# Performance work log

Hardware: AMD Instinct MI355X
Metric: run time of the kernel (lower is better)

## Reference

```python
import jax, jax.numpy as jnp
import numpy as np

E = 64          # num experts
CAP = 64        # tokens per expert (uniform routing)
H = 1024        # hidden_size
F = 2048        # ffn_hidden_size


def setup_inputs() -> dict:
    key = jax.random.key(0)
    k1, k2, k3 = jax.random.split(key, 3)
    x = jax.random.normal(k1, (E * CAP, H), dtype=jnp.float32)
    # dMoE stores expert weights flattened as [E*F, H]
    w1 = jax.random.normal(k2, (E * F, H), dtype=jnp.float32) * 0.02
    w2 = jax.random.normal(k3, (E * F, H), dtype=jnp.float32) * 0.02
    return {"x": x, "w1": w1, "w2": w2, "num_experts": E}


def reference(x, w1, w2, num_experts):
    # Block-sparse sdd/dsd over a block-diagonal expert topology is a grouped GEMM:
    # tokens are sorted by expert; each group of CAP tokens hits one expert's weights.
    T, Hd = x.shape
    Fd = w1.shape[0] // num_experts
    cap = T // num_experts
    xg = x.reshape(num_experts, cap, Hd)            # [E, cap, H]
    w1g = w1.reshape(num_experts, Fd, Hd)           # [E, F, H]
    w2g = w2.reshape(num_experts, Fd, Hd)           # [E, F, H]
    # sdd: x @ w1^T restricted to expert blocks
    h = jnp.einsum('ech,efh->ecf', xg, w1g)         # [E, cap, F]
    # megablocks' gelu kernel uses the tanh approximation
    h = jax.nn.gelu(h, approximate=True)
    # dsd: h @ w2 restricted to expert blocks
    out = jnp.einsum('ecf,efh->ech', h, w2g)        # [E, cap, H]
    return out.reshape(T, Hd)
```

## Files before the change

### kernel.cpp

```cpp
#include <hip/hip_runtime.h>


typedef __attribute__((ext_vector_type(8))) short short8;
typedef __attribute__((ext_vector_type(4))) float f32x4;
typedef __attribute__((ext_vector_type(8))) unsigned short ushort8;

#define NE   64
#define CAPT 64
#define HD   1024
#define FD   2048

__device__ __forceinline__ unsigned short f2bf(float f) {
  union { float f; unsigned u; } v; v.f = f;
  unsigned r = v.u + 0x7FFFu + ((v.u >> 16) & 1u);
  return (unsigned short)(r >> 16);
}

__device__ __forceinline__ float gelu_t(float v) {
  float u = 0.7978845608028654f * (v + 0.044715f * v * v * v);
  return 0.5f * v * (1.0f + tanhf(u));
}

__device__ __forceinline__ int swz(int row, int kbyte) {
  return row * 128 + (kbyte ^ ((row & 7) << 4));
}

__device__ __forceinline__ void cvt_wr4(unsigned char* dst, float4 v) {
  uint2 p;
  p.x = (unsigned)f2bf(v.x) | ((unsigned)f2bf(v.y) << 16);
  p.y = (unsigned)f2bf(v.z) | ((unsigned)f2bf(v.w) << 16);
  *(uint2*)dst = p;
}

__global__ __launch_bounds__(512, 4)
void moe_pass1(const float* __restrict__ x, const float* __restrict__ w1,
               unsigned short* __restrict__ hb) {
  __shared__ __align__(16) unsigned char sA[64 * 128];
  __shared__ __align__(16) unsigned char sB[128 * 128];
  const int e = blockIdx.x >> 4, nb = blockIdx.x & 15;
  const int t = threadIdx.x, lane = t & 63, wid = t >> 6;
  const int wm = wid >> 2, wn = wid & 3;
  const int lr = lane & 15, lkb = (lane >> 4) * 16;

  const float* xg  = x  + (size_t)e * CAPT * HD;
  const float* w1g = w1 + ((size_t)e * FD + (size_t)nb * 128) * HD;

  f32x4 acc[2][2] = {};

  float4 ra[2], rb[4];
  auto loadT = [&](int k0) {
    #pragma unroll
    for (int i = 0; i < 2; ++i) {
      int u = t + i * 512;
      ra[i] = *(const float4*)(xg + (u >> 4) * HD + k0 + (u & 15) * 4);
    }
    #pragma unroll
    for (int i = 0; i < 4; ++i) {
      int u = t + i * 512;
      rb[i] = *(const float4*)(w1g + (u >> 4) * HD + k0 + (u & 15) * 4);
    }
  };

  loadT(0);
  for (int ks = 0; ks < HD / 64; ++ks) {
    __syncthreads();
    #pragma unroll
    for (int i = 0; i < 2; ++i) {
      int u = t + i * 512;
      cvt_wr4(sA + swz(u >> 4, (u & 15) * 8), ra[i]);
    }
    #pragma unroll
    for (int i = 0; i < 4; ++i) {
      int u = t + i * 512;
      cvt_wr4(sB + swz(u >> 4, (u & 15) * 8), rb[i]);
    }
    __syncthreads();
    if (ks + 1 < HD / 64) loadT((ks + 1) * 64);

    short8 af[2][2], bf[2][2];
    #pragma unroll
    for (int fm = 0; fm < 2; ++fm)
      #pragma unroll
      for (int kk = 0; kk < 2; ++kk) {
        int row = wm * 32 + fm * 16 + lr;
        af[fm][kk] = *(const short8*)(sA + swz(row, kk * 64 + lkb));
      }
    #pragma unroll
    for (int fn = 0; fn < 2; ++fn)
      #pragma unroll
      for (int kk = 0; kk < 2; ++kk) {
        int row = wn * 32 + fn * 16 + lr;
        bf[fn][kk] = *(const short8*)(sB + swz(row, kk * 64 + lkb));
      }
    #pragma unroll
    for (int fm = 0; fm < 2; ++fm)
      #pragma unroll
      for (int fn = 0; fn < 2; ++fn) {
        acc[fm][fn] = __builtin_amdgcn_mfma_f32_16x16x32_bf16(af[fm][0], bf[fn][0], acc[fm][fn], 0, 0, 0);
        acc[fm][fn] = __builtin_amdgcn_mfma_f32_16x16x32_bf16(af[fm][1], bf[fn][1], acc[fm][fn], 0, 0, 0);
      }
  }

  unsigned short* hp = hb + (size_t)e * CAPT * FD + nb * 128;
  #pragma unroll
  for (int fm = 0; fm < 2; ++fm)
    #pragma unroll
    for (int fn = 0; fn < 2; ++fn)
      #pragma unroll
      for (int j = 0; j < 4; ++j) {
        int m = wm * 32 + fm * 16 + (lane >> 4) * 4 + j;
        int f = wn * 32 + fn * 16 + lr;
        hp[(size_t)m * FD + f] = f2bf(gelu_t(acc[fm][fn][j]));
      }
}

__global__ __launch_bounds__(512, 4)
void moe_pass2(const unsigned short* __restrict__ hb, const float* __restrict__ w2,
               float* __restrict__ out) {
  __shared__ __align__(16) unsigned char sA[64 * 128];
  __shared__ __align__(16) unsigned char sB[128 * 128];
  const int e = blockIdx.x >> 3, nb = blockIdx.x & 7;
  const int t = threadIdx.x, lane = t & 63, wid = t >> 6;
  const int wm = wid >> 2, wn = wid & 3;
  const int lr = lane & 15, lkb = (lane >> 4) * 16;

  const unsigned short* hg = hb + (size_t)e * CAPT * FD;
  const float* w2g = w2 + (size_t)e * FD * HD + nb * 128;

  f32x4 acc[2][2] = {};

  const int ar = t >> 3, ac = t & 7;
  const int bn = t & 127, bkg = t >> 7;

  ushort8 rav;
  float rbv[16];
  auto loadT = [&](int f0) {
    rav = *(const ushort8*)(hg + (size_t)ar * FD + f0 + ac * 8);
    #pragma unroll
    for (int i = 0; i < 4; ++i)
      #pragma unroll
      for (int j = 0; j < 4; ++j)
        rbv[i * 4 + j] = w2g[(size_t)(f0 + bkg * 16 + i * 4 + j) * HD + bn];
  };

  loadT(0);
  for (int ks = 0; ks < FD / 64; ++ks) {
    __syncthreads();
    *(ushort8*)(sA + swz(ar, ac * 16)) = rav;
    #pragma unroll
    for (int i = 0; i < 4; ++i) {
      uint2 p;
      p.x = (unsigned)f2bf(rbv[i * 4 + 0]) | ((unsigned)f2bf(rbv[i * 4 + 1]) << 16);
      p.y = (unsigned)f2bf(rbv[i * 4 + 2]) | ((unsigned)f2bf(rbv[i * 4 + 3]) << 16);
      *(uint2*)(sB + swz(bn, (bkg * 16 + i * 4) * 2)) = p;
    }
    __syncthreads();
    if (ks + 1 < FD / 64) loadT((ks + 1) * 64);

    short8 af[2][2], bf[2][2];
    #pragma unroll
    for (int fm = 0; fm < 2; ++fm)
      #pragma unroll
      for (int kk = 0; kk < 2; ++kk) {
        int row = wm * 32 + fm * 16 + lr;
        af[fm][kk] = *(const short8*)(sA + swz(row, kk * 64 + lkb));
      }
    #pragma unroll
    for (int fn = 0; fn < 2; ++fn)
      #pragma unroll
      for (int kk = 0; kk < 2; ++kk) {
        int row = wn * 32 + fn * 16 + lr;
        bf[fn][kk] = *(const short8*)(sB + swz(row, kk * 64 + lkb));
      }
    #pragma unroll
    for (int fm = 0; fm < 2; ++fm)
      #pragma unroll
      for (int fn = 0; fn < 2; ++fn) {
        acc[fm][fn] = __builtin_amdgcn_mfma_f32_16x16x32_bf16(af[fm][0], bf[fn][0], acc[fm][fn], 0, 0, 0);
        acc[fm][fn] = __builtin_amdgcn_mfma_f32_16x16x32_bf16(af[fm][1], bf[fn][1], acc[fm][fn], 0, 0, 0);
      }
  }

  float* op = out + (size_t)e * CAPT * HD + nb * 128;
  #pragma unroll
  for (int fm = 0; fm < 2; ++fm)
    #pragma unroll
    for (int fn = 0; fn < 2; ++fn)
      #pragma unroll
      for (int j = 0; j < 4; ++j) {
        int m = wm * 32 + fm * 16 + (lane >> 4) * 4 + j;
        int n = wn * 32 + fn * 16 + lr;
        op[(size_t)m * HD + n] = acc[fm][fn][j];
      }
}

extern "C" void kernel_launch(void* const* d_in, const int* in_sizes, int n_in,
                              void* d_out, int out_size, void* d_ws, size_t ws_size,
                              hipStream_t stream) {
  const float* x  = (const float*)d_in[0];
  const float* w1 = (const float*)d_in[1];
  const float* w2 = (const float*)d_in[2];
  float* out = (float*)d_out;
  unsigned short* hb = (unsigned short*)d_ws;
  (void)in_sizes; (void)n_in; (void)out_size; (void)ws_size;

  moe_pass1<<<dim3(NE * (FD / 128)), dim3(512), 0, stream>>>(x, w1, hb);
  moe_pass2<<<dim3(NE * (HD / 128)), dim3(512), 0, stream>>>(hb, w2, out);
}
```

Baseline: 234.3 us.

## Double-buffer LDS tiles in both GEMM passes and use an exp-based GELU

Both grouped-GEMM kernels now keep two LDS buffers. The next tile is converted and written to the idle buffer while MFMAs read the current one, so each k-step needs one barrier instead of two, and global loads are issued two steps ahead. The tanh GELU is rewritten algebraically as v*sigmoid(2u) using __expf, which is cheaper than tanhf. The cost is double the LDS per block (48KB), which may lower occupancy against the requested 4 blocks per CU, and more registers held live across iterations.

```diff
diff --git a/kernel.cpp b/kernel.cpp
--- a/kernel.cpp
+++ b/kernel.cpp
@@ -17,8 +17,8 @@
 }
 
 __device__ __forceinline__ float gelu_t(float v) {
-  float u = 0.7978845608028654f * (v + 0.044715f * v * v * v);
-  return 0.5f * v * (1.0f + tanhf(u));
+  float u = 1.5957691216057308f * (v + 0.044715f * v * v * v);
+  return v / (1.0f + __expf(-u));
 }
 
 __device__ __forceinline__ int swz(int row, int kbyte) {
@@ -32,11 +32,14 @@
   *(uint2*)dst = p;
 }
 
+#define A_SZ (64 * 128)
+#define B_SZ (128 * 128)
+
 __global__ __launch_bounds__(512, 4)
 void moe_pass1(const float* __restrict__ x, const float* __restrict__ w1,
                unsigned short* __restrict__ hb) {
-  __shared__ __align__(16) unsigned char sA[64 * 128];
-  __shared__ __align__(16) unsigned char sB[128 * 128];
+  __shared__ __align__(16) unsigned char sA[2 * A_SZ];
+  __shared__ __align__(16) unsigned char sB[2 * B_SZ];
   const int e = blockIdx.x >> 4, nb = blockIdx.x & 15;
   const int t = threadIdx.x, lane = t & 63, wid = t >> 6;
   const int wm = wid >> 2, wn = wid & 3;
@@ -60,38 +63,43 @@
       rb[i] = *(const float4*)(w1g + (u >> 4) * HD + k0 + (u & 15) * 4);
     }
   };
-
+  auto writeT = [&](unsigned char* a, unsigned char* b) {
+    #pragma unroll
+    for (int i = 0; i < 2; ++i) {
+      int u = t + i * 512;
+      cvt_wr4(a + swz(u >> 4, (u & 15) * 8), ra[i]);
+    }
+    #pragma unroll
+    for (int i = 0; i < 4; ++i) {
+      int u = t + i * 512;
+      cvt_wr4(b + swz(u >> 4, (u & 15) * 8), rb[i]);
+    }
+  };
+
+  const int NK = HD / 64;
   loadT(0);
-  for (int ks = 0; ks < HD / 64; ++ks) {
-    __syncthreads();
-    #pragma unroll
-    for (int i = 0; i < 2; ++i) {
-      int u = t + i * 512;
-      cvt_wr4(sA + swz(u >> 4, (u & 15) * 8), ra[i]);
-    }
-    #pragma unroll
-    for (int i = 0; i < 4; ++i) {
-      int u = t + i * 512;
-      cvt_wr4(sB + swz(u >> 4, (u & 15) * 8), rb[i]);
-    }
-    __syncthreads();
-    if (ks + 1 < HD / 64) loadT((ks + 1) * 64);
+  writeT(sA, sB);
+  loadT(64);
+  __syncthreads();
+
+  int cur = 0;
+  for (int ks = 0; ks < NK; ++ks) {
+    unsigned char* cA = sA + cur * A_SZ;
+    unsigned char* cB = sB + cur * B_SZ;
+    if (ks + 1 < NK) writeT(sA + (cur ^ 1) * A_SZ, sB + (cur ^ 1) * B_SZ);
+    if (ks + 2 < NK) loadT((ks + 2) * 64);
 
     short8 af[2][2], bf[2][2];
     #pragma unroll
     for (int fm = 0; fm < 2; ++fm)
       #pragma unroll
-      for (int kk = 0; kk < 2; ++kk) {
-        int row = wm * 32 + fm * 16 + lr;
-        af[fm][kk] = *(const short8*)(sA + swz(row, kk * 64 + lkb));
-      }
-    #pragma unroll
-    for (int fn = 0; fn < 2; ++fn)
-      #pragma unroll
-      for (int kk = 0; kk < 2; ++kk) {
-        int row = wn * 32 + fn * 16 + lr;
-        bf[fn][kk] = *(const short8*)(sB + swz(row, kk * 64 + lkb));
-      }
+      for (int kk = 0; kk < 2; ++kk)
+        af[fm][kk] = *(const short8*)(cA + swz(wm * 32 + fm * 16 + lr, kk * 64 + lkb));
+    #pragma unroll
+    for (int fn = 0; fn < 2; ++fn)
+      #pragma unroll
+      for (int kk = 0; kk < 2; ++kk)
+        bf[fn][kk] = *(const short8*)(cB + swz(wn * 32 + fn * 16 + lr, kk * 64 + lkb));
     #pragma unroll
     for (int fm = 0; fm < 2; ++fm)
       #pragma unroll
@@ -99,6 +107,8 @@
         acc[fm][fn] = __builtin_amdgcn_mfma_f32_16x16x32_bf16(af[fm][0], bf[fn][0], acc[fm][fn], 0, 0, 0);
         acc[fm][fn] = __builtin_amdgcn_mfma_f32_16x16x32_bf16(af[fm][1], bf[fn][1], acc[fm][fn], 0, 0, 0);
       }
+    __syncthreads();
+    cur ^= 1;
   }
 
   unsigned short* hp = hb + (size_t)e * CAPT * FD + nb * 128;
@@ -117,8 +127,8 @@
 __global__ __launch_bounds__(512, 4)
 void moe_pass2(const unsigned short* __restrict__ hb, const float* __restrict__ w2,
                float* __restrict__ out) {
-  __shared__ __align__(16) unsigned char sA[64 * 128];
-  __shared__ __align__(16) unsigned char sB[128 * 128];
+  __shared__ __align__(16) unsigned char sA[2 * A_SZ];
+  __shared__ __align__(16) unsigned char sB[2 * B_SZ];
   const int e = blockIdx.x >> 3, nb = blockIdx.x & 7;
   const int t = threadIdx.x, lane = t & 63, wid = t >> 6;
   const int wm = wid >> 2, wn = wid & 3;
@@ -142,36 +152,41 @@
       for (int j = 0; j < 4; ++j)
         rbv[i * 4 + j] = w2g[(size_t)(f0 + bkg * 16 + i * 4 + j) * HD + bn];
   };
-
-  loadT(0);
-  for (int ks = 0; ks < FD / 64; ++ks) {
-    __syncthreads();
-    *(ushort8*)(sA + swz(ar, ac * 16)) = rav;
+  auto writeT = [&](unsigned char* a, unsigned char* b) {
+    *(ushort8*)(a + swz(ar, ac * 16)) = rav;
     #pragma unroll
     for (int i = 0; i < 4; ++i) {
       uint2 p;
       p.x = (unsigned)f2bf(rbv[i * 4 + 0]) | ((unsigned)f2bf(rbv[i * 4 + 1]) << 16);
       p.y = (unsigned)f2bf(rbv[i * 4 + 2]) | ((unsigned)f2bf(rbv[i * 4 + 3]) << 16);
-      *(uint2*)(sB + swz(bn, (bkg * 16 + i * 4) * 2)) = p;
-    }
-    __syncthreads();
-    if (ks + 1 < FD / 64) loadT((ks + 1) * 64);
+      *(uint2*)(b + swz(bn, (bkg * 16 + i * 4) * 2)) = p;
+    }
+  };
+
+  const int NK = FD / 64;
+  loadT(0);
+  writeT(sA, sB);
+  loadT(64);
+  __syncthreads();
+
+  int cur = 0;
+  for (int ks = 0; ks < NK; ++ks) {
+    unsigned char* cA = sA + cur * A_SZ;
+    unsigned char* cB = sB + cur * B_SZ;
+    if (ks + 1 < NK) writeT(sA + (cur ^ 1) * A_SZ, sB + (cur ^ 1) * B_SZ);
+    if (ks + 2 < NK) loadT((ks + 2) * 64);
 
     short8 af[2][2], bf[2][2];
     #pragma unroll
     for (int fm = 0; fm < 2; ++fm)
       #pragma unroll
-      for (int kk = 0; kk < 2; ++kk) {
-        int row = wm * 32 + fm * 16 + lr;
-        af[fm][kk] = *(const short8*)(sA + swz(row, kk * 64 + lkb));
-      }
-    #pragma unroll
-    for (int fn = 0; fn < 2; ++fn)
-      #pragma unroll
-      for (int kk = 0; kk < 2; ++kk) {
-        int row = wn * 32 + fn * 16 + lr;
-        bf[fn][kk] = *(const short8*)(sB + swz(row, kk * 64 + lkb));
-      }
+      for (int kk = 0; kk < 2; ++kk)
+        af[fm][kk] = *(const short8*)(cA + swz(wm * 32 + fm * 16 + lr, kk * 64 + lkb));
+    #pragma unroll
+    for (int fn = 0; fn < 2; ++fn)
+      #pragma unroll
+      for (int kk = 0; kk < 2; ++kk)
+        bf[fn][kk] = *(const short8*)(cB + swz(wn * 32 + fn * 16 + lr, kk * 64 + lkb));
     #pragma unroll
     for (int fm = 0; fm < 2; ++fm)
       #pragma unroll
@@ -179,6 +194,8 @@
         acc[fm][fn] = __builtin_amdgcn_mfma_f32_16x16x32_bf16(af[fm][0], bf[fn][0], acc[fm][fn], 0, 0, 0);
         acc[fm][fn] = __builtin_amdgcn_mfma_f32_16x16x32_bf16(af[fm][1], bf[fn][1], acc[fm][fn], 0, 0, 0);
       }
+    __syncthreads();
+    cur ^= 1;
   }
 
   float* op = out + (size_t)e * CAPT * HD + nb * 128;
```

Result: no change. 230.9 us (-1.4%).
